# Optimization experiments

Measured on AMD Instinct MI355X. Metric: run time of the kernel, lower is better.

The kernel has to match this reference:

```python
import jax, jax.numpy as jnp
import numpy as np
from jax import lax

B, C, H, W = 16, 256, 64, 64
EXP = 2
C2 = C * EXP  # expanded channels
EPS = 1e-5


def setup_inputs() -> dict:
    key = jax.random.key(0)
    ks = jax.random.split(key, 8)
    def he(k, shape, fan_out):
        return jax.random.normal(k, shape, jnp.float32) * np.sqrt(2.0 / fan_out)
    return {
        "f": jax.random.normal(ks[0], (B, C, H, W), jnp.float32),
        "ln_gamma": jnp.ones((C,), jnp.float32),
        "ln_beta": jnp.zeros((C,), jnp.float32),
        "w_expand": he(ks[1], (C2, C), C2),          # 1x1 conv [out,in]
        "freq_real": jnp.ones((C2,), jnp.float32),
        "freq_imag": jnp.zeros((C2,), jnp.float32),
        "w_poly": he(ks[2], (C2, C2), C2),
        "w_dw": he(ks[3], (C2, 1, 3, 3), 9),          # depthwise 3x3, fan_out=1*3*3
        "w_pw": he(ks[4], (C2, C2), C2),
        "w_final": he(ks[5], (C, C2), C),
    }


def reference(f, ln_gamma, ln_beta, w_expand, freq_real, freq_imag,
              w_poly, w_dw, w_pw, w_final):
    # LayerNorm over channel dim (torch permutes to NHWC, norms last dim)
    mu = jnp.mean(f, axis=1, keepdims=True)
    var = jnp.var(f, axis=1, keepdims=True)
    f1 = (f - mu) * lax.rsqrt(var + EPS)
    f1 = f1 * ln_gamma[None, :, None, None] + ln_beta[None, :, None, None]
    # 1x1 expand
    f2 = jnp.einsum('bchw,oc->bohw', f1, w_expand)
    # FFT2 -> multiply by per-channel complex scalar (r + i*j) -> IFFT2 -> real.
    # Since the filter is constant over all frequencies and f2 is real, this is
    # exactly Re((r+i*j) * f2) = r * f2; freq_imag contributes nothing.
    f4 = f2 * freq_real[None, :, None, None]
    # polymerize 1x1
    f5 = jnp.einsum('bchw,oc->bohw', f4, w_poly)
    # depthwise 3x3, SAME padding
    f6 = lax.conv_general_dilated(
        f5, w_dw, window_strides=(1, 1), padding='SAME',
        dimension_numbers=('NCHW', 'OIHW', 'NCHW'), feature_group_count=C2)
    # pointwise 1x1
    f6 = jnp.einsum('bchw,oc->bohw', f6, w_pw)
    # GELU (exact erf, torch default) gating
    f7 = jax.nn.gelu(f6, approximate=False) * f6
    # 1x1 reduce + residual
    f8 = jnp.einsum('bchw,oc->bohw', f7, w_final)
    return f + f8
```

## Files before the change

kernel.cpp:

```cpp
#include <hip/hip_runtime.h>
#include <hip/hip_bf16.h>
#include <math.h>

#define Bn 16
#define Cc 256
#define Hh 64
#define Ww 64
#define HW 4096
#define C2 512
#define Pp 65536
#define EPSc 1e-5f

typedef __attribute__((ext_vector_type(8))) short short8;
typedef __attribute__((ext_vector_type(4))) float floatx4;

__global__ __launch_bounds__(256)
void combine_weights(const float* __restrict__ w_expand,
                     const float* __restrict__ freq_real,
                     const float* __restrict__ w_poly,
                     const float* __restrict__ gamma,
                     const float* __restrict__ beta,
                     __hip_bfloat16* __restrict__ W1g_b,
                     float* __restrict__ bias1,
                     float* __restrict__ wsum) {
    int o = blockIdx.x;
    int c = threadIdx.x;
    float acc = 0.f;
    const float* wp = w_poly + (size_t)o * C2;
    for (int m = 0; m < C2; ++m) {
        acc += wp[m] * freq_real[m] * w_expand[(size_t)m * Cc + c];
    }
    float wg = acc * gamma[c];
    W1g_b[(size_t)o * Cc + c] = __float2bfloat16(wg);
    __shared__ float redB[256];
    __shared__ float redG[256];
    redB[c] = acc * beta[c];
    redG[c] = wg;
    __syncthreads();
    for (int s = 128; s > 0; s >>= 1) {
        if (c < s) { redB[c] += redB[c + s]; redG[c] += redG[c + s]; }
        __syncthreads();
    }
    if (c == 0) { bias1[o] = redB[0]; wsum[o] = redG[0]; }
}

__global__ __launch_bounds__(256)
void to_bf16(const float* __restrict__ a, __hip_bfloat16* __restrict__ o, int n) {
    int i = (blockIdx.x * 256 + threadIdx.x) * 4;
    if (i < n) {
        float4 v = *(const float4*)&a[i];
        __hip_bfloat16 r[4];
        r[0] = __float2bfloat16(v.x);
        r[1] = __float2bfloat16(v.y);
        r[2] = __float2bfloat16(v.z);
        r[3] = __float2bfloat16(v.w);
        *(uint2*)&o[i] = *(const uint2*)r;
    }
}

__global__ __launch_bounds__(256)
void pad_dw(const float* __restrict__ w_dw, float* __restrict__ w_dw_p) {
    int i = blockIdx.x * 256 + threadIdx.x;
    if (i < C2 * 12) {
        int k = i / 12, j = i - k * 12;
        w_dw_p[i] = (j < 9) ? w_dw[k * 9 + j] : 0.f;
    }
}

#define XP 264

__global__ __launch_bounds__(256, 3)
void prep_x(const float* __restrict__ f,
            __hip_bfloat16* __restrict__ x_bf,
            float* __restrict__ muA,
            float* __restrict__ rsA) {
    __shared__ __hip_bfloat16 Bs[64 * XP];
    __shared__ float redS[1024], redQ[1024];

    int blk = blockIdx.x;
    int b = blk >> 6;
    int s0 = (blk & 63) << 6;
    int tid = threadIdx.x;
    int x = tid & 15, g = tid >> 4;

    const float* fb = f + (size_t)b * Cc * HW + s0 + x * 4;

    float4 v0r[8], v1r[8];
#pragma unroll
    for (int it = 0; it < 8; ++it) {
        int c = (it * 16 + g) * 2;
        v0r[it] = *(const float4*)&fb[(size_t)c * HW];
        v1r[it] = *(const float4*)&fb[(size_t)(c + 1) * HW];
    }

    float lsum[4] = {0.f, 0.f, 0.f, 0.f};
    float lsq[4]  = {0.f, 0.f, 0.f, 0.f};
    unsigned* dst = (unsigned*)&Bs[0];
#pragma unroll
    for (int it = 0; it < 8; ++it) {
        int cpair = it * 16 + g;
        float a0[4] = {v0r[it].x, v0r[it].y, v0r[it].z, v0r[it].w};
        float a1[4] = {v1r[it].x, v1r[it].y, v1r[it].z, v1r[it].w};
#pragma unroll
        for (int j = 0; j < 4; ++j) {
            lsum[j] += a0[j] + a1[j];
            lsq[j]  += a0[j] * a0[j] + a1[j] * a1[j];
            __hip_bfloat16 b0 = __float2bfloat16(a0[j]);
            __hip_bfloat16 b1 = __float2bfloat16(a1[j]);
            unsigned pk = ((unsigned)__bfloat16_as_ushort(b1) << 16) |
                          (unsigned)__bfloat16_as_ushort(b0);
            dst[(size_t)(x * 4 + j) * (XP / 2) + cpair] = pk;
        }
    }
#pragma unroll
    for (int j = 0; j < 4; ++j) {
        redS[g * 64 + x * 4 + j] = lsum[j];
        redQ[g * 64 + x * 4 + j] = lsq[j];
    }
    __syncthreads();

    if (tid < 64) {
        float s = 0.f, q = 0.f;
#pragma unroll
        for (int gg = 0; gg < 16; ++gg) {
            s += redS[gg * 64 + tid];
            q += redQ[gg * 64 + tid];
        }
        float m = s * (1.0f / 256.0f);
        int p = blk * 64 + tid;
        muA[p] = m;
        rsA[p] = rsqrtf(q * (1.0f / 256.0f) - m * m + EPSc);
    }

    int n = tid >> 2, q4 = tid & 3;
    const __hip_bfloat16* src = &Bs[(size_t)n * XP + q4 * 64];
    __hip_bfloat16* gout = x_bf + ((size_t)blk * 64 + n) * Cc + q4 * 64;
#pragma unroll
    for (int i = 0; i < 8; ++i)
        *(uint4*)&gout[i * 8] = *(const uint4*)&src[i * 8];
}

__global__ __launch_bounds__(256, 3)
void gemm1b(const __hip_bfloat16* __restrict__ x_bf,
            const __hip_bfloat16* __restrict__ W1g_b,
            const float* __restrict__ bias1,
            const float* __restrict__ wsum,
            const float* __restrict__ muA,
            const float* __restrict__ rsA,
            __hip_bfloat16* __restrict__ f5) {
    __shared__ __hip_bfloat16 As[128 * 32];
    __shared__ __hip_bfloat16 Ws[128 * 32];

    int flat = blockIdx.x;
    int ct = flat & 3;
    int pt = flat >> 2;
    int p0 = pt * 128, c0 = ct * 128;
    int tid = threadIdx.x;
    int lane = tid & 63, wave = tid >> 6;
    int col = lane & 15, quad = lane >> 4;
    int wp = wave >> 1, wc = wave & 1;

    floatx4 acc[4][4];
#pragma unroll
    for (int i = 0; i < 4; ++i)
#pragma unroll
        for (int j = 0; j < 4; ++j)
            acc[i][j] = (floatx4){0.f, 0.f, 0.f, 0.f};

    int row0 = tid >> 2, part0 = tid & 3;
    int idx1 = 256 + tid;
    int row1 = idx1 >> 2, part1 = idx1 & 3;

    for (int ks = 0; ks < 8; ++ks) {
        int k0 = ks * 32;
        uint4 ga0 = *(const uint4*)&x_bf[((size_t)(p0 + row0)) * Cc + k0 + part0 * 8];
        uint4 ga1 = *(const uint4*)&x_bf[((size_t)(p0 + row1)) * Cc + k0 + part1 * 8];
        uint4 gb0 = *(const uint4*)&W1g_b[((size_t)(c0 + row0)) * Cc + k0 + part0 * 8];
        uint4 gb1 = *(const uint4*)&W1g_b[((size_t)(c0 + row1)) * Cc + k0 + part1 * 8];
        if (ks > 0) __syncthreads();
        *(uint4*)&As[(size_t)row0 * 32 + part0 * 8] = ga0;
        *(uint4*)&As[(size_t)row1 * 32 + part1 * 8] = ga1;
        *(uint4*)&Ws[(size_t)row0 * 32 + part0 * 8] = gb0;
        *(uint4*)&Ws[(size_t)row1 * 32 + part1 * 8] = gb1;
        __syncthreads();

        short8 af[4], bf[4];
#pragma unroll
        for (int i = 0; i < 4; ++i)
            af[i] = *(const short8*)&As[(size_t)(wp * 64 + i * 16 + col) * 32 + quad * 8];
#pragma unroll
        for (int j = 0; j < 4; ++j)
            bf[j] = *(const short8*)&Ws[(size_t)(wc * 64 + j * 16 + col) * 32 + quad * 8];
#pragma unroll
        for (int i = 0; i < 4; ++i)
#pragma unroll
            for (int j = 0; j < 4; ++j)
                acc[i][j] = __builtin_amdgcn_mfma_f32_16x16x32_bf16(af[i], bf[j], acc[i][j], 0, 0, 0);
    }

    int b2 = p0 >> 12;
    int sbase = p0 & 4095;
#pragma unroll
    for (int i = 0; i < 4; ++i) {
        int pl = wp * 64 + i * 16 + quad * 4;
        float4 mu4 = *(const float4*)&muA[p0 + pl];
        float4 rs4 = *(const float4*)&rsA[p0 + pl];
        float mu_[4] = {mu4.x, mu4.y, mu4.z, mu4.w};
        float rs_[4] = {rs4.x, rs4.y, rs4.z, rs4.w};
#pragma unroll
        for (int j = 0; j < 4; ++j) {
            int c = c0 + wc * 64 + j * 16 + col;
            float ws_ = wsum[c], bi_ = bias1[c];
            __hip_bfloat16 v4[4];
#pragma unroll
            for (int r = 0; r < 4; ++r) {
                float v = (acc[i][j][r] - mu_[r] * ws_) * rs_[r] + bi_;
                v4[r] = __float2bfloat16(v);
            }
            *(uint2*)&f5[((size_t)b2 * C2 + c) * HW + sbase + pl] = *(const uint2*)v4;
        }
    }
}

#define TPITCH 520

__global__ __launch_bounds__(512, 4)
void fused_tail(const __hip_bfloat16* __restrict__ f5,
                const float* __restrict__ w_dw_p,
                const __hip_bfloat16* __restrict__ w_pw_b,
                const __hip_bfloat16* __restrict__ w_final_b,
                const float* __restrict__ f,
                float* __restrict__ out) {
    __shared__ __hip_bfloat16 tT[64 * TPITCH];

    int flat = blockIdx.x;
    int xcd = flat & 7;
    int slot = flat >> 3;
    int hb = slot & 7;
    int b  = slot >> 3;
    int h  = xcd * 8 + hb;

    int tid = threadIdx.x;
    int lane = tid & 63;
    int wave = tid >> 6;
    int col = lane & 15;
    int quad = lane >> 4;

    const __hip_bfloat16* f5b = f5 + (size_t)b * C2 * HW;
    int t4 = tid & 3;
    int kb = tid >> 2;
    int w16 = t4 * 16;

    uint4 curC[3][2], nxtC[3][2];
#pragma unroll
    for (int dy = 0; dy < 3; ++dy) {
        int hh = h + dy - 1;
        if ((unsigned)hh < Hh) {
            const __hip_bfloat16* row = f5b + (size_t)kb * HW + hh * Ww + w16;
            curC[dy][0] = *(const uint4*)&row[0];
            curC[dy][1] = *(const uint4*)&row[8];
        } else {
            curC[dy][0] = make_uint4(0, 0, 0, 0);
            curC[dy][1] = make_uint4(0, 0, 0, 0);
        }
    }

#pragma unroll
    for (int it = 0; it < 4; ++it) {
        int k = it * 128 + kb;
        if (it < 3) {
            int k2 = k + 128;
#pragma unroll
            for (int dy = 0; dy < 3; ++dy) {
                int hh = h + dy - 1;
                if ((unsigned)hh < Hh) {
                    const __hip_bfloat16* row = f5b + (size_t)k2 * HW + hh * Ww + w16;
                    nxtC[dy][0] = *(const uint4*)&row[0];
                    nxtC[dy][1] = *(const uint4*)&row[8];
                } else {
                    nxtC[dy][0] = make_uint4(0, 0, 0, 0);
                    nxtC[dy][1] = make_uint4(0, 0, 0, 0);
                }
            }
        }
        const float4* wd4 = (const float4*)(w_dw_p + (size_t)k * 12);
        float4 wa = wd4[0], wb = wd4[1], wc2 = wd4[2];
        float wreg[9] = {wa.x, wa.y, wa.z, wa.w, wb.x, wb.y, wb.z, wb.w, wc2.x};
        float acc16[16] = {};
#pragma unroll
        for (int dy = 0; dy < 3; ++dy) {
            const __hip_bfloat16* pv = (const __hip_bfloat16*)&curC[dy][0];
            float cv[16];
#pragma unroll
            for (int j = 0; j < 16; ++j) cv[j] = __bfloat162float(pv[j]);
            float l_in = __shfl_up(cv[15], 1);
            float r_in = __shfl_down(cv[0], 1);
            if (t4 == 0) l_in = 0.f;
            if (t4 == 3) r_in = 0.f;
            float win[18];
            win[0] = l_in;
#pragma unroll
            for (int j = 0; j < 16; ++j) win[j + 1] = cv[j];
            win[17] = r_in;
#pragma unroll
            for (int j = 0; j < 16; ++j)
                acc16[j] += wreg[dy * 3 + 0] * win[j] +
                            wreg[dy * 3 + 1] * win[j + 1] +
                            wreg[dy * 3 + 2] * win[j + 2];
        }
#pragma unroll
        for (int j = 0; j < 16; ++j)
            tT[(size_t)(w16 + j) * TPITCH + k] = __float2bfloat16(acc16[j]);
        if (it < 3) {
#pragma unroll
            for (int dy = 0; dy < 3; ++dy) {
                curC[dy][0] = nxtC[dy][0];
                curC[dy][1] = nxtC[dy][1];
            }
        }
    }

    int wm0 = wave * 64;
    const __hip_bfloat16* Ap = w_pw_b + (size_t)(wm0 + col) * C2 + quad * 8;
    short8 a_cur[4], a_nxt[4];
#pragma unroll
    for (int mt = 0; mt < 4; ++mt)
        a_cur[mt] = *(const short8*)(Ap + (size_t)mt * 16 * C2);

    __syncthreads();

    floatx4 acc[4][4];
#pragma unroll
    for (int mt = 0; mt < 4; ++mt)
#pragma unroll
        for (int nt = 0; nt < 4; ++nt)
            acc[mt][nt] = (floatx4){0.f, 0.f, 0.f, 0.f};

#pragma unroll
    for (int ks = 0; ks < 16; ++ks) {
        int k0 = ks * 32;
        if (ks < 15) {
#pragma unroll
            for (int mt = 0; mt < 4; ++mt)
                a_nxt[mt] = *(const short8*)(Ap + (size_t)mt * 16 * C2 + k0 + 32);
        }
        short8 bfr[4];
#pragma unroll
        for (int nt = 0; nt < 4; ++nt)
            bfr[nt] = *(const short8*)&tT[(size_t)(nt * 16 + col) * TPITCH + k0 + quad * 8];
#pragma unroll
        for (int mt = 0; mt < 4; ++mt)
#pragma unroll
            for (int nt = 0; nt < 4; ++nt)
                acc[mt][nt] = __builtin_amdgcn_mfma_f32_16x16x32_bf16(a_cur[mt], bfr[nt], acc[mt][nt], 0, 0, 0);
        if (ks < 15) {
#pragma unroll
            for (int mt = 0; mt < 4; ++mt) a_cur[mt] = a_nxt[mt];
        }
    }
    __syncthreads();

#pragma unroll
    for (int mt = 0; mt < 4; ++mt)
#pragma unroll
        for (int nt = 0; nt < 4; ++nt) {
            __hip_bfloat16 v4[4];
#pragma unroll
            for (int r = 0; r < 4; ++r) {
                float v = acc[mt][nt][r];
                float gl = 0.5f * v * (1.0f + erff(v * 0.70710678118f));
                v4[r] = __float2bfloat16(gl * v);
            }
            *(uint2*)&tT[(size_t)(nt * 16 + col) * TPITCH + wm0 + mt * 16 + quad * 4] = *(const uint2*)v4;
        }

    int wm2 = wave * 32;
    const __hip_bfloat16* Af = w_final_b + (size_t)(wm2 + col) * C2 + quad * 8;
    short8 c_cur[2], c_nxt[2];
#pragma unroll
    for (int mt = 0; mt < 2; ++mt)
        c_cur[mt] = *(const short8*)(Af + (size_t)mt * 16 * C2);

    const float* fb = f + (size_t)b * Cc * HW + h * Ww;
    float* ob = out + (size_t)b * Cc * HW + h * Ww;
    float fres[2][4][4];
#pragma unroll
    for (int mt = 0; mt < 2; ++mt)
#pragma unroll
        for (int nt = 0; nt < 4; ++nt)
#pragma unroll
            for (int r = 0; r < 4; ++r) {
                int m = wm2 + mt * 16 + quad * 4 + r;
                int n = nt * 16 + col;
                fres[mt][nt][r] = fb[(size_t)m * HW + n];
            }

    __syncthreads();

    floatx4 acc2[2][4];
#pragma unroll
    for (int mt = 0; mt < 2; ++mt)
#pragma unroll
        for (int nt = 0; nt < 4; ++nt)
            acc2[mt][nt] = (floatx4){0.f, 0.f, 0.f, 0.f};

#pragma unroll
    for (int ks = 0; ks < 16; ++ks) {
        int k0 = ks * 32;
        if (ks < 15) {
#pragma unroll
            for (int mt = 0; mt < 2; ++mt)
                c_nxt[mt] = *(const short8*)(Af + (size_t)mt * 16 * C2 + k0 + 32);
        }
        short8 bfr[4];
#pragma unroll
        for (int nt = 0; nt < 4; ++nt)
            bfr[nt] = *(const short8*)&tT[(size_t)(nt * 16 + col) * TPITCH + k0 + quad * 8];
#pragma unroll
        for (int mt = 0; mt < 2; ++mt)
#pragma unroll
            for (int nt = 0; nt < 4; ++nt)
                acc2[mt][nt] = __builtin_amdgcn_mfma_f32_16x16x32_bf16(c_cur[mt], bfr[nt], acc2[mt][nt], 0, 0, 0);
        if (ks < 15) {
#pragma unroll
            for (int mt = 0; mt < 2; ++mt) c_cur[mt] = c_nxt[mt];
        }
    }

#pragma unroll
    for (int mt = 0; mt < 2; ++mt)
#pragma unroll
        for (int nt = 0; nt < 4; ++nt)
#pragma unroll
            for (int r = 0; r < 4; ++r) {
                int m = wm2 + mt * 16 + quad * 4 + r;
                int n = nt * 16 + col;
                ob[(size_t)m * HW + n] = fres[mt][nt][r] + acc2[mt][nt][r];
            }
}

extern "C" void kernel_launch(void* const* d_in, const int* in_sizes, int n_in,
                              void* d_out, int out_size, void* d_ws, size_t ws_size,
                              hipStream_t stream) {
    const float* f         = (const float*)d_in[0];
    const float* ln_gamma  = (const float*)d_in[1];
    const float* ln_beta   = (const float*)d_in[2];
    const float* w_expand  = (const float*)d_in[3];
    const float* freq_real = (const float*)d_in[4];
    const float* w_poly    = (const float*)d_in[6];
    const float* w_dw      = (const float*)d_in[7];
    const float* w_pw      = (const float*)d_in[8];
    const float* w_final   = (const float*)d_in[9];
    float* out = (float*)d_out;

    char* p = (char*)d_ws;
    __hip_bfloat16* f5   = (__hip_bfloat16*)p;  p += (size_t)C2 * Pp * 2;
    __hip_bfloat16* x_bf = (__hip_bfloat16*)p;  p += (size_t)Cc * Pp * 2;
    __hip_bfloat16* W1g_b = (__hip_bfloat16*)p; p += (size_t)C2 * Cc * 2;
    float* bias1 = (float*)p;                   p += (size_t)C2 * 4;
    float* wsum  = (float*)p;                   p += (size_t)C2 * 4;
    float* muA   = (float*)p;                   p += (size_t)Pp * 4;
    float* rsA   = (float*)p;                   p += (size_t)Pp * 4;
    __hip_bfloat16* w_pw_b    = (__hip_bfloat16*)p;  p += (size_t)C2 * C2 * 2;
    __hip_bfloat16* w_final_b = (__hip_bfloat16*)p;  p += (size_t)Cc * C2 * 2;
    float* w_dw_p = (float*)p;                  p += (size_t)C2 * 12 * 4;

    combine_weights<<<dim3(C2), dim3(256), 0, stream>>>(
        w_expand, freq_real, w_poly, ln_gamma, ln_beta, W1g_b, bias1, wsum);

    to_bf16<<<dim3((C2 * C2 / 4 + 255) / 256), dim3(256), 0, stream>>>(
        w_pw, w_pw_b, C2 * C2);
    to_bf16<<<dim3((Cc * C2 / 4 + 255) / 256), dim3(256), 0, stream>>>(
        w_final, w_final_b, Cc * C2);
    pad_dw<<<dim3((C2 * 12 + 255) / 256), dim3(256), 0, stream>>>(w_dw, w_dw_p);

    prep_x<<<dim3(Pp / 64), dim3(256), 0, stream>>>(f, x_bf, muA, rsA);

    gemm1b<<<dim3(2048), dim3(256), 0, stream>>>(
        x_bf, W1g_b, bias1, wsum, muA, rsA, f5);

    fused_tail<<<dim3(1024), dim3(512), 0, stream>>>(
        f5, w_dw_p, w_pw_b, w_final_b, f, out);
}
```

Before: 373.7 us.

## Fuse LayerNorm stats and bf16 transpose into first GEMM kernel

Merges prep_x and gemm1b into one kernel. Each 512-thread block loads a 64-pixel fp32 tile of f, computes per-pixel channel mean and rstd in shared memory, transposes the tile to bf16 in LDS, and runs the 64x512 GEMM against the combined weights. Weight fragments are read straight from global memory with register double-buffering instead of being staged in LDS. This removes the x_bf, muA and rsA round-trips through global memory and one launch. In exchange, every block re-reads the full weight matrix from global or L2, and each block now covers 64 pixels instead of 128.

```diff
diff --git a/kernel.cpp b/kernel.cpp
--- a/kernel.cpp
+++ b/kernel.cpp
@@ -67,98 +67,75 @@
     }
 }
 
-#define XP 264
-
-__global__ __launch_bounds__(256, 3)
-void prep_x(const float* __restrict__ f,
-            __hip_bfloat16* __restrict__ x_bf,
-            float* __restrict__ muA,
-            float* __restrict__ rsA) {
-    __shared__ __hip_bfloat16 Bs[64 * XP];
-    __shared__ float redS[1024], redQ[1024];
-
-    int blk = blockIdx.x;
-    int b = blk >> 6;
-    int s0 = (blk & 63) << 6;
+#define XPAD 264
+
+__global__ __launch_bounds__(512, 4)
+void gemm1f(const float* __restrict__ f,
+            const __hip_bfloat16* __restrict__ W1g_b,
+            const float* __restrict__ bias1,
+            const float* __restrict__ wsum,
+            __hip_bfloat16* __restrict__ f5) {
+    __shared__ __hip_bfloat16 As[64 * XPAD];
+    __shared__ float redS[32 * 64];
+    __shared__ float redQ[32 * 64];
+    __shared__ float muS[64];
+    __shared__ float rsS[64];
+
+    int flat = blockIdx.x;
+    int b = flat >> 6;
+    int h = flat & 63;
+    int s0 = h * 64;
+
     int tid = threadIdx.x;
-    int x = tid & 15, g = tid >> 4;
+    int x = tid & 15;
+    int cg = tid >> 4;
 
     const float* fb = f + (size_t)b * Cc * HW + s0 + x * 4;
-
-    float4 v0r[8], v1r[8];
-#pragma unroll
-    for (int it = 0; it < 8; ++it) {
-        int c = (it * 16 + g) * 2;
-        v0r[it] = *(const float4*)&fb[(size_t)c * HW];
-        v1r[it] = *(const float4*)&fb[(size_t)(c + 1) * HW];
-    }
+    unsigned* Asu = (unsigned*)&As[0];
 
     float lsum[4] = {0.f, 0.f, 0.f, 0.f};
     float lsq[4]  = {0.f, 0.f, 0.f, 0.f};
-    unsigned* dst = (unsigned*)&Bs[0];
-#pragma unroll
-    for (int it = 0; it < 8; ++it) {
-        int cpair = it * 16 + g;
-        float a0[4] = {v0r[it].x, v0r[it].y, v0r[it].z, v0r[it].w};
-        float a1[4] = {v1r[it].x, v1r[it].y, v1r[it].z, v1r[it].w};
+#pragma unroll
+    for (int i = 0; i < 4; ++i) {
+        int cp = i * 32 + cg;
+        float4 v0 = *(const float4*)&fb[(size_t)(cp * 2) * HW];
+        float4 v1 = *(const float4*)&fb[(size_t)(cp * 2 + 1) * HW];
+        float a0[4] = {v0.x, v0.y, v0.z, v0.w};
+        float a1[4] = {v1.x, v1.y, v1.z, v1.w};
 #pragma unroll
         for (int j = 0; j < 4; ++j) {
             lsum[j] += a0[j] + a1[j];
             lsq[j]  += a0[j] * a0[j] + a1[j] * a1[j];
-            __hip_bfloat16 b0 = __float2bfloat16(a0[j]);
-            __hip_bfloat16 b1 = __float2bfloat16(a1[j]);
-            unsigned pk = ((unsigned)__bfloat16_as_ushort(b1) << 16) |
-                          (unsigned)__bfloat16_as_ushort(b0);
-            dst[(size_t)(x * 4 + j) * (XP / 2) + cpair] = pk;
+            unsigned pk = ((unsigned)__bfloat16_as_ushort(__float2bfloat16(a1[j])) << 16)
+                        |  (unsigned)__bfloat16_as_ushort(__float2bfloat16(a0[j]));
+            Asu[(size_t)(x * 4 + j) * (XPAD / 2) + cp] = pk;
         }
     }
 #pragma unroll
     for (int j = 0; j < 4; ++j) {
-        redS[g * 64 + x * 4 + j] = lsum[j];
-        redQ[g * 64 + x * 4 + j] = lsq[j];
-    }
-    __syncthreads();
-
+        redS[cg * 64 + x * 4 + j] = lsum[j];
+        redQ[cg * 64 + x * 4 + j] = lsq[j];
+    }
+
+    int lane = tid & 63, wave = tid >> 6;
+    int col = lane & 15, quad = lane >> 4;
+    int c0w = wave * 64;
+    const __hip_bfloat16* Bp = W1g_b + (size_t)(c0w + col) * Cc + quad * 8;
+    short8 b_cur[4], b_nxt[4];
+#pragma unroll
+    for (int j = 0; j < 4; ++j)
+        b_cur[j] = *(const short8*)(Bp + (size_t)j * 16 * Cc);
+
+    __syncthreads();
     if (tid < 64) {
         float s = 0.f, q = 0.f;
 #pragma unroll
-        for (int gg = 0; gg < 16; ++gg) {
-            s += redS[gg * 64 + tid];
-            q += redQ[gg * 64 + tid];
-        }
+        for (int g = 0; g < 32; ++g) { s += redS[g * 64 + tid]; q += redQ[g * 64 + tid]; }
         float m = s * (1.0f / 256.0f);
-        int p = blk * 64 + tid;
-        muA[p] = m;
-        rsA[p] = rsqrtf(q * (1.0f / 256.0f) - m * m + EPSc);
-    }
-
-    int n = tid >> 2, q4 = tid & 3;
-    const __hip_bfloat16* src = &Bs[(size_t)n * XP + q4 * 64];
-    __hip_bfloat16* gout = x_bf + ((size_t)blk * 64 + n) * Cc + q4 * 64;
-#pragma unroll
-    for (int i = 0; i < 8; ++i)
-        *(uint4*)&gout[i * 8] = *(const uint4*)&src[i * 8];
-}
-
-__global__ __launch_bounds__(256, 3)
-void gemm1b(const __hip_bfloat16* __restrict__ x_bf,
-            const __hip_bfloat16* __restrict__ W1g_b,
-            const float* __restrict__ bias1,
-            const float* __restrict__ wsum,
-            const float* __restrict__ muA,
-            const float* __restrict__ rsA,
-            __hip_bfloat16* __restrict__ f5) {
-    __shared__ __hip_bfloat16 As[128 * 32];
-    __shared__ __hip_bfloat16 Ws[128 * 32];
-
-    int flat = blockIdx.x;
-    int ct = flat & 3;
-    int pt = flat >> 2;
-    int p0 = pt * 128, c0 = ct * 128;
-    int tid = threadIdx.x;
-    int lane = tid & 63, wave = tid >> 6;
-    int col = lane & 15, quad = lane >> 4;
-    int wp = wave >> 1, wc = wave & 1;
+        muS[tid] = m;
+        rsS[tid] = rsqrtf(q * (1.0f / 256.0f) - m * m + EPSc);
+    }
+    __syncthreads();
 
     floatx4 acc[4][4];
 #pragma unroll
@@ -167,49 +144,40 @@
         for (int j = 0; j < 4; ++j)
             acc[i][j] = (floatx4){0.f, 0.f, 0.f, 0.f};
 
-    int row0 = tid >> 2, part0 = tid & 3;
-    int idx1 = 256 + tid;
-    int row1 = idx1 >> 2, part1 = idx1 & 3;
-
+#pragma unroll
     for (int ks = 0; ks < 8; ++ks) {
         int k0 = ks * 32;
-        uint4 ga0 = *(const uint4*)&x_bf[((size_t)(p0 + row0)) * Cc + k0 + part0 * 8];
-        uint4 ga1 = *(const uint4*)&x_bf[((size_t)(p0 + row1)) * Cc + k0 + part1 * 8];
-        uint4 gb0 = *(const uint4*)&W1g_b[((size_t)(c0 + row0)) * Cc + k0 + part0 * 8];
-        uint4 gb1 = *(const uint4*)&W1g_b[((size_t)(c0 + row1)) * Cc + k0 + part1 * 8];
-        if (ks > 0) __syncthreads();
-        *(uint4*)&As[(size_t)row0 * 32 + part0 * 8] = ga0;
-        *(uint4*)&As[(size_t)row1 * 32 + part1 * 8] = ga1;
-        *(uint4*)&Ws[(size_t)row0 * 32 + part0 * 8] = gb0;
-        *(uint4*)&Ws[(size_t)row1 * 32 + part1 * 8] = gb1;
-        __syncthreads();
-
-        short8 af[4], bf[4];
+        if (ks < 7) {
+#pragma unroll
+            for (int j = 0; j < 4; ++j)
+                b_nxt[j] = *(const short8*)(Bp + (size_t)j * 16 * Cc + k0 + 32);
+        }
+        short8 af[4];
 #pragma unroll
         for (int i = 0; i < 4; ++i)
-            af[i] = *(const short8*)&As[(size_t)(wp * 64 + i * 16 + col) * 32 + quad * 8];
-#pragma unroll
-        for (int j = 0; j < 4; ++j)
-            bf[j] = *(const short8*)&Ws[(size_t)(wc * 64 + j * 16 + col) * 32 + quad * 8];
+            af[i] = *(const short8*)&As[(size_t)(i * 16 + col) * XPAD + k0 + quad * 8];
 #pragma unroll
         for (int i = 0; i < 4; ++i)
 #pragma unroll
             for (int j = 0; j < 4; ++j)
-                acc[i][j] = __builtin_amdgcn_mfma_f32_16x16x32_bf16(af[i], bf[j], acc[i][j], 0, 0, 0);
-    }
-
-    int b2 = p0 >> 12;
-    int sbase = p0 & 4095;
+                acc[i][j] = __builtin_amdgcn_mfma_f32_16x16x32_bf16(af[i], b_cur[j], acc[i][j], 0, 0, 0);
+        if (ks < 7) {
+#pragma unroll
+            for (int j = 0; j < 4; ++j) b_cur[j] = b_nxt[j];
+        }
+    }
+
+    __hip_bfloat16* f5b = f5 + (size_t)b * C2 * HW + s0;
 #pragma unroll
     for (int i = 0; i < 4; ++i) {
-        int pl = wp * 64 + i * 16 + quad * 4;
-        float4 mu4 = *(const float4*)&muA[p0 + pl];
-        float4 rs4 = *(const float4*)&rsA[p0 + pl];
+        int pl = i * 16 + quad * 4;
+        float4 mu4 = *(const float4*)&muS[pl];
+        float4 rs4 = *(const float4*)&rsS[pl];
         float mu_[4] = {mu4.x, mu4.y, mu4.z, mu4.w};
         float rs_[4] = {rs4.x, rs4.y, rs4.z, rs4.w};
 #pragma unroll
         for (int j = 0; j < 4; ++j) {
-            int c = c0 + wc * 64 + j * 16 + col;
+            int c = c0w + j * 16 + col;
             float ws_ = wsum[c], bi_ = bias1[c];
             __hip_bfloat16 v4[4];
 #pragma unroll
@@ -217,7 +185,7 @@
                 float v = (acc[i][j][r] - mu_[r] * ws_) * rs_[r] + bi_;
                 v4[r] = __float2bfloat16(v);
             }
-            *(uint2*)&f5[((size_t)b2 * C2 + c) * HW + sbase + pl] = *(const uint2*)v4;
+            *(uint2*)&f5b[(size_t)c * HW + pl] = *(const uint2*)v4;
         }
     }
 }
@@ -455,12 +423,9 @@
 
     char* p = (char*)d_ws;
     __hip_bfloat16* f5   = (__hip_bfloat16*)p;  p += (size_t)C2 * Pp * 2;
-    __hip_bfloat16* x_bf = (__hip_bfloat16*)p;  p += (size_t)Cc * Pp * 2;
     __hip_bfloat16* W1g_b = (__hip_bfloat16*)p; p += (size_t)C2 * Cc * 2;
     float* bias1 = (float*)p;                   p += (size_t)C2 * 4;
     float* wsum  = (float*)p;                   p += (size_t)C2 * 4;
-    float* muA   = (float*)p;                   p += (size_t)Pp * 4;
-    float* rsA   = (float*)p;                   p += (size_t)Pp * 4;
     __hip_bfloat16* w_pw_b    = (__hip_bfloat16*)p;  p += (size_t)C2 * C2 * 2;
     __hip_bfloat16* w_final_b = (__hip_bfloat16*)p;  p += (size_t)Cc * C2 * 2;
     float* w_dw_p = (float*)p;                  p += (size_t)C2 * 12 * 4;
@@ -474,10 +439,8 @@
         w_final, w_final_b, Cc * C2);
     pad_dw<<<dim3((C2 * 12 + 255) / 256), dim3(256), 0, stream>>>(w_dw, w_dw_p);
 
-    prep_x<<<dim3(Pp / 64), dim3(256), 0, stream>>>(f, x_bf, muA, rsA);
-
-    gemm1b<<<dim3(2048), dim3(256), 0, stream>>>(
-        x_bf, W1g_b, bias1, wsum, muA, rsA, f5);
+    gemm1f<<<dim3(1024), dim3(512), 0, stream>>>(
+        f, W1g_b, bias1, wsum, f5);
 
     fused_tail<<<dim3(1024), dim3(512), 0, stream>>>(
         f5, w_dw_p, w_pw_b, w_final_b, f, out);
```

New measurement: 362.0 us. 3.1% less time.
